# Kernel optimization log

Hardware: AMD Instinct MI355X
Metric: run time of the kernel (lower is better)

Reference implementation:

```python
import jax, jax.numpy as jnp
import numpy as np

T, B, N, E, NF, L = 4, 8, 5000, 80000, 16, 3


def setup_inputs() -> dict:
    key = jax.random.key(0)
    ks = jax.random.split(key, 12)
    xs = jax.random.normal(ks[0], (T, B, N, 3), jnp.float32)
    vs = jax.random.normal(ks[1], (T, B, N, 3), jnp.float32)
    charges = jax.random.uniform(ks[2], (B * N, 1), jnp.float32)
    edge_src = jax.random.randint(ks[3], (E,), 0, N)
    edge_dst = jax.random.randint(ks[4], (E,), 0, N)
    theta = jax.random.uniform(ks[5], (1, T), jnp.float32, -1.0, 1.0)  # uniform_(-1,1)
    W_embed = jax.random.normal(ks[6], (1, NF), jnp.float32) * 0.5
    W1 = jax.random.normal(ks[7], (L, 2 * NF + 1, NF), jnp.float32) / jnp.sqrt(2.0 * NF + 1)
    b1 = jnp.zeros((L, NF), jnp.float32)
    W2 = jax.random.normal(ks[8], (L, NF, NF), jnp.float32) / jnp.sqrt(float(NF))
    b2 = jnp.zeros((L, NF), jnp.float32)
    Wv = jax.random.normal(ks[9], (L, NF, 1), jnp.float32) * 0.1
    return dict(xs=xs, vs=vs, charges=charges, edge_src=edge_src, edge_dst=edge_dst,
                theta=theta, W_embed=W_embed, W1=W1, b1=b1, W2=W2, b2=b2, Wv=Wv)


def reference(xs, vs, charges, edge_src, edge_dst, theta, W_embed, W1, b1, W2, b2, Wv):
    T_, B_, N_, _ = xs.shape
    # node scalar features ('f' / type-0) initialized from charges
    h0 = jax.nn.relu(charges.reshape(B_, N_, 1) @ W_embed)  # [B, N, NF]

    def graph_step(x, v, h):
        # x, v: [N,3]; h: [N,NF]. Equivariant message passing with edge rel-pos gather.
        d = x[edge_dst] - x[edge_src]                      # [E,3]  (edata['d'])
        d2 = jnp.sum(d * d, axis=-1, keepdims=True)        # [E,1]  invariant edge feature
        vec = v                                            # type-1 ('vel') channel
        for l in range(L):
            feat = jnp.concatenate([h[edge_src], h[edge_dst], d2], axis=-1)  # [E,2NF+1]
            m = jax.nn.relu(feat @ W1[l] + b1[l])                            # [E,NF]
            agg = jax.ops.segment_sum(m, edge_dst, num_segments=N_)          # [N,NF]
            h = h + jax.nn.relu(agg @ W2[l] + b2[l])
            # equivariant vector update: scatter d-weighted messages
            vec = vec + jax.ops.segment_sum(d * (m @ Wv[l]), edge_dst, num_segments=N_)
        return vec + x  # module returns out + xs

    step_b = jax.vmap(graph_step)                                  # over batch
    out = jax.vmap(lambda x, v: step_b(x, v, h0))(xs, vs)          # [T,B,N,3]
    x = out.reshape(T_, B_ * N_, 3)                                # step's view(-1, 3)
    x_hat = jnp.einsum('ij,jkt->ikt', jax.nn.softmax(theta, axis=1), x)
    return x_hat.squeeze(0)  # [B*N, 3] since num_future == 1
```

## Files before the change

### kernel.cpp

```cpp
#include <hip/hip_runtime.h>
#include <hip/hip_bf16.h>

constexpr int T_ = 4;
constexpr int B_ = 8;
constexpr int N_ = 5000;
constexpr int E_ = 80000;
constexpr int TBN = T_ * B_ * N_;
constexpr int NXCD = 8;
constexpr int CAP = 64;

constexpr int NPB = 32;
constexpr int CH  = (N_ + NPB - 1) / NPB;
constexpr int GRP = T_ * B_ / NXCD;
constexpr int LB  = NXCD * CH * GRP;
constexpr int EB  = (E_ + 255) / 256;
constexpr int IB  = TBN / 256;


__device__ __forceinline__ unsigned bf16pack2(float lo, float hi) {
    unsigned ul = (__float_as_uint(lo) + 0x8000u) >> 16;
    unsigned uh = (__float_as_uint(hi) + 0x8000u) & 0xffff0000u;
    return uh | ul;
}
__device__ __forceinline__ void bf16unpack2(unsigned u, float& lo, float& hi) {
    lo = __uint_as_float(u << 16);
    hi = __uint_as_float(u & 0xffff0000u);
}

__global__ void k_build(const int* __restrict__ src, const int* __restrict__ dst,
                        int* __restrict__ cursor, unsigned short* __restrict__ csr_b,
                        const float* __restrict__ xs, const float* __restrict__ vs,
                        const float* __restrict__ charges,
                        float4* __restrict__ rec0, float4* __restrict__ rec1,
                        float* __restrict__ vec) {
    const int bid = blockIdx.x;
    const int tid = threadIdx.x;
    if (bid < EB) {
        int e = bid * 256 + tid;
        if (e < E_) {
            int d = dst[e];
            int pos = atomicAdd(&cursor[d], 1);
            if (pos < CAP) csr_b[d * CAP + pos] = (unsigned short)src[e];
        }
    } else {
        int g = (bid - EB) * 256 + tid;
        int tb = g / N_;
        int n  = g - tb * N_;
        int b  = tb % B_;
        float c = charges[b * N_ + n];
        float4 xc = make_float4(xs[3*(size_t)g], xs[3*(size_t)g+1], xs[3*(size_t)g+2], c);
        rec0[(size_t)g * 3 + 2] = xc;
        rec1[(size_t)g * 3 + 2] = xc;
        vec[3*(size_t)g+0] = vs[3*(size_t)g+0];
        vec[3*(size_t)g+1] = vs[3*(size_t)g+1];
        vec[3*(size_t)g+2] = vs[3*(size_t)g+2];
    }
}

template <int LYR, bool HAS_NEXT>
__global__ __launch_bounds__(256, 6) void k_layer(
        const float4* __restrict__ rec_in, float4* __restrict__ rec_out,
        const float* __restrict__ W_embed,
        const float* __restrict__ W1, const float* __restrict__ b1,
        const float* __restrict__ W2, const float* __restrict__ b2,
        const float* __restrict__ Wv, const float* __restrict__ theta,
        const int* __restrict__ degv, const unsigned short* __restrict__ csr_b,
        unsigned* __restrict__ hbuf, unsigned* __restrict__ gd,
        float* __restrict__ vec, float* __restrict__ outp) {
    __shared__ float s_w1e[16], s_wv[16], s_b2[16], s_b1[16], s_b1n[16];
    __shared__ float s_W2[256];
    __shared__ float s_W1sn[256];
    __shared__ float s_W1dn[256];
    __shared__ float s_P[16], s_Q[16], s_rwe[16];
    const int tid = threadIdx.x;
    if (tid < 16) {
        s_w1e[tid] = W1[LYR * 528 + 512 + tid];
        s_wv[tid]  = Wv[LYR * 16 + tid];
        s_b2[tid]  = b2[LYR * 16 + tid];
        s_b1[tid]  = b1[LYR * 16 + tid];
        if (HAS_NEXT) s_b1n[tid] = b1[(LYR + 1) * 16 + tid];
    }
    s_W2[tid] = W2[LYR * 256 + tid];
    if (HAS_NEXT) {
        s_W1sn[tid] = W1[(LYR + 1) * 528 + tid];
        s_W1dn[tid] = W1[(LYR + 1) * 528 + 256 + tid];
    }
    if (LYR == 0 && tid < 16) {
        float accP = 0.0f, accQ = 0.0f;
        for (int j = 0; j < 16; ++j) {
            float r = fmaxf(W_embed[j], 0.0f);
            accP += r * W1[j * 16 + tid];
            accQ += r * W1[256 + j * 16 + tid];
        }
        s_P[tid] = accP; s_Q[tid] = accQ;
        s_rwe[tid] = fmaxf(W_embed[tid], 0.0f);
    }
    __syncthreads();

    const int bid   = blockIdx.x;
    const int xcd   = bid & 7;
    const int j     = bid >> 3;
    const int tb    = xcd + NXCD * (j / CH);
    const int chunk = j % CH;
    const int o     = tid & 7;
    const int node  = chunk * NPB + (tid >> 3);
    const int half  = o & 1;
    const int pr    = o >> 1;
    const int hb    = half * 8;
    if (node >= N_) return;

    const int g = tb * N_ + node;
    const size_t nb = (size_t)tb * N_;
    const uint4* r4 = (const uint4*)rec_in;

    float wsm = 0.0f;
    if (!HAS_NEXT) {
        float t0 = theta[0], t1 = theta[1], t2 = theta[2], t3 = theta[3];
        float mx = fmaxf(fmaxf(t0, t1), fmaxf(t2, t3));
        float e0 = expf(t0 - mx), e1 = expf(t1 - mx);
        float e2 = expf(t2 - mx), e3 = expf(t3 - mx);
        float inv = 1.0f / (e0 + e1 + e2 + e3);
        int tt = tb >> 3;
        wsm = ((tt == 0) ? e0 : (tt == 1) ? e1 : (tt == 2) ? e2 : e3) * inv;
    }

    const float4 xn = rec_in[(size_t)g * 3 + 2];
    const float c0 = xn.w;

    float gdn[8];
    if (LYR == 0) {
#pragma unroll
        for (int k = 0; k < 8; ++k) gdn[k] = c0 * s_Q[hb + k] + s_b1[hb + k];
    } else {
        uint4 da = ((const uint4*)gd)[(size_t)g * 2 + half];
        bf16unpack2(da.x, gdn[0], gdn[1]);  bf16unpack2(da.y, gdn[2], gdn[3]);
        bf16unpack2(da.z, gdn[4], gdn[5]);  bf16unpack2(da.w, gdn[6], gdn[7]);
    }

    float agg[8];
#pragma unroll
    for (int k = 0; k < 8; ++k) agg[k] = 0.0f;
    float av0 = 0.0f, av1 = 0.0f, av2 = 0.0f;

    const int deg = min(degv[node], CAP);
    const int rs = node * CAP;
    const int re = rs + deg;

    int e = rs + pr;
    bool have = e < re;
    int s = have ? (int)csr_b[e] : 0;
    size_t si = nb + (size_t)s;
    float4 xc = rec_in[si * 3 + 2];
    uint4  ga;
    if (LYR != 0) ga = r4[si * 3 + half];

    while (have) {
        int e2 = e + 4;
        bool have2 = e2 < re;
        int s2 = have2 ? (int)csr_b[e2] : 0;
        size_t si2 = nb + (size_t)s2;
        float4 xc2 = rec_in[si2 * 3 + 2];
        uint4  ga2;
        if (LYR != 0) ga2 = r4[si2 * 3 + half];

        float d0 = xn.x - xc.x;
        float d1 = xn.y - xc.y;
        float d2v = xn.z - xc.z;
        float dd = d0*d0 + d1*d1 + d2v*d2v;

        float gsf[8];
        if (LYR == 0) {
            float cs = xc.w;
#pragma unroll
            for (int k = 0; k < 8; ++k) gsf[k] = cs * s_P[hb + k];
        } else {
            bf16unpack2(ga.x, gsf[0], gsf[1]);  bf16unpack2(ga.y, gsf[2], gsf[3]);
            bf16unpack2(ga.z, gsf[4], gsf[5]);  bf16unpack2(ga.w, gsf[6], gsf[7]);
        }

        float sval = 0.0f;
#pragma unroll
        for (int k = 0; k < 8; ++k) {
            float mv = fmaxf(__builtin_fmaf(dd, s_w1e[hb + k], gdn[k]) + gsf[k], 0.0f);
            if (HAS_NEXT) agg[k] += mv;
            sval = __builtin_fmaf(mv, s_wv[hb + k], sval);
        }
        sval += __shfl_xor(sval, 1);
        av0 = __builtin_fmaf(d0, sval, av0);
        av1 = __builtin_fmaf(d1, sval, av1);
        av2 = __builtin_fmaf(d2v, sval, av2);

        e = e2; have = have2; xc = xc2; ga = ga2;
    }

    av0 += __shfl_xor(av0, 2); av0 += __shfl_xor(av0, 4);
    av1 += __shfl_xor(av1, 2); av1 += __shfl_xor(av1, 4);
    av2 += __shfl_xor(av2, 2); av2 += __shfl_xor(av2, 4);

    if (HAS_NEXT) {
        if (o < 3) {
            float myav = (o == 0) ? av0 : ((o == 1) ? av1 : av2);
            vec[(size_t)g * 3 + o] += myav;
        }

#pragma unroll
        for (int k = 0; k < 8; ++k) {
            agg[k] += __shfl_xor(agg[k], 2);
            agg[k] += __shfl_xor(agg[k], 4);
        }
        float aggO[8];
#pragma unroll
        for (int k = 0; k < 8; ++k) aggO[k] = __shfl_xor(agg[k], 1);
        const int j0 = hb;
        const int j1 = 8 - hb;

        float hq0, hq1;
        if (LYR == 0) {
            hq0 = c0 * s_rwe[o * 2];
            hq1 = c0 * s_rwe[o * 2 + 1];
        } else {
            bf16unpack2(hbuf[(size_t)g * 8 + o], hq0, hq1);
        }

        float a0 = s_b2[o * 2], a1 = s_b2[o * 2 + 1];
#pragma unroll
        for (int k = 0; k < 8; ++k) {
            a0 = __builtin_fmaf(agg[k],  s_W2[(j0 + k) * 16 + o * 2],     a0);
            a1 = __builtin_fmaf(agg[k],  s_W2[(j0 + k) * 16 + o * 2 + 1], a1);
            a0 = __builtin_fmaf(aggO[k], s_W2[(j1 + k) * 16 + o * 2],     a0);
            a1 = __builtin_fmaf(aggO[k], s_W2[(j1 + k) * 16 + o * 2 + 1], a1);
        }
        hq0 += fmaxf(a0, 0.0f);
        hq1 += fmaxf(a1, 0.0f);

        const int lane = tid & 63;
        const int lbase = lane & ~7;
        float hfull[16];
#pragma unroll
        for (int sq = 0; sq < 8; ++sq) {
            hfull[sq * 2]     = __shfl(hq0, lbase + sq, 64);
            hfull[sq * 2 + 1] = __shfl(hq1, lbase + sq, 64);
        }

        float gs0 = 0.0f, gs1 = 0.0f;
        float gd0 = s_b1n[o * 2], gd1 = s_b1n[o * 2 + 1];
#pragma unroll
        for (int jj = 0; jj < 16; ++jj) {
            float hj = hfull[jj];
            gs0 = __builtin_fmaf(hj, s_W1sn[jj * 16 + o * 2],     gs0);
            gs1 = __builtin_fmaf(hj, s_W1sn[jj * 16 + o * 2 + 1], gs1);
            gd0 = __builtin_fmaf(hj, s_W1dn[jj * 16 + o * 2],     gd0);
            gd1 = __builtin_fmaf(hj, s_W1dn[jj * 16 + o * 2 + 1], gd1);
        }

        hbuf[(size_t)g * 8 + o] = bf16pack2(hq0, hq1);
        ((unsigned*)rec_out)[(size_t)g * 12 + o] = bf16pack2(gs0, gs1);
        ((unsigned*)gd)[(size_t)g * 8 + o]       = bf16pack2(gd0, gd1);
    } else {
        if (o < 3) {
            float myav = (o == 0) ? av0 : ((o == 1) ? av1 : av2);
            float xno  = (o == 0) ? xn.x : ((o == 1) ? xn.y : xn.z);
            float prev = vec[(size_t)g * 3 + o];
            int b = tb & 7;
            atomicAdd(&outp[((size_t)b * N_ + node) * 3 + o],
                      wsm * (prev + myav + xno));
        }
    }
}

extern "C" void kernel_launch(void* const* d_in, const int* in_sizes, int n_in,
                              void* d_out, int out_size, void* d_ws, size_t ws_size,
                              hipStream_t stream) {
    const float* xs       = (const float*)d_in[0];
    const float* vs       = (const float*)d_in[1];
    const float* charges  = (const float*)d_in[2];
    const int*   edge_src = (const int*)d_in[3];
    const int*   edge_dst = (const int*)d_in[4];
    const float* theta    = (const float*)d_in[5];
    const float* W_embed  = (const float*)d_in[6];
    const float* W1       = (const float*)d_in[7];
    const float* b1       = (const float*)d_in[8];
    const float* W2       = (const float*)d_in[9];
    const float* b2       = (const float*)d_in[10];
    const float* Wv       = (const float*)d_in[11];
    float* out = (float*)d_out;

    char* w = (char*)d_ws;
    size_t off = 0;
    auto take = [&](size_t bytes) {
        size_t o = off;
        off = (off + bytes + 255) & ~(size_t)255;
        return o;
    };
    int*            cursor = (int*)(w + take((size_t)N_ * 4));
    unsigned short* csr_b  = (unsigned short*)(w + take((size_t)N_ * CAP * 2));
    float4*         rec0   = (float4*)(w + take((size_t)TBN * 48));
    float4*         rec1   = (float4*)(w + take((size_t)TBN * 48));
    unsigned*       hbuf   = (unsigned*)(w + take((size_t)TBN * 32));
    unsigned*       gd     = (unsigned*)(w + take((size_t)TBN * 32));
    float*          vec    = (float*)(w + take((size_t)TBN * 3 * 4));
    (void)ws_size;

    hipMemsetAsync(cursor, 0, (size_t)N_ * 4, stream);
    hipMemsetAsync(out, 0, (size_t)out_size * 4, stream);
    k_build<<<EB + IB, 256, 0, stream>>>(edge_src, edge_dst, cursor, csr_b,
                                         xs, vs, charges, rec0, rec1, vec);

    k_layer<0, true ><<<LB, 256, 0, stream>>>(rec0, rec1, W_embed, W1, b1, W2, b2, Wv,
                                              theta, cursor, csr_b, hbuf, gd, vec, out);
    k_layer<1, true ><<<LB, 256, 0, stream>>>(rec1, rec0, W_embed, W1, b1, W2, b2, Wv,
                                              theta, cursor, csr_b, hbuf, gd, vec, out);
    k_layer<2, false><<<LB, 256, 0, stream>>>(rec0, nullptr, W_embed, W1, b1, W2, b2, Wv,
                                              theta, cursor, csr_b, hbuf, gd, vec, out);
}
```

Measured before the change: 106.8 us.

## Quantize positions/charges to int16 and stage whole graph in LDS

Positions and charges are quantized once into 8-byte fixed-point records. Each layer block copies all 5000 node records for its graph into shared memory, so neighbor position gathers read LDS instead of global memory. The gs records shrink from a 48-byte interleaved layout to a separate 32-byte array, and blocks grow to 512 threads handling 64 nodes each. The trade-offs are fixed-point precision loss on positions, about 40KB of LDS per block that limits occupancy, and a per-block load of the whole graph that is repeated across chunks.

```diff
diff --git a/kernel.cpp b/kernel.cpp
--- a/kernel.cpp
+++ b/kernel.cpp
@@ -9,13 +9,18 @@
 constexpr int NXCD = 8;
 constexpr int CAP = 64;
 
-constexpr int NPB = 32;
+constexpr int TPB = 512;
+constexpr int NPB = 64;
 constexpr int CH  = (N_ + NPB - 1) / NPB;
 constexpr int GRP = T_ * B_ / NXCD;
 constexpr int LB  = NXCD * CH * GRP;
 constexpr int EB  = (E_ + 255) / 256;
 constexpr int IB  = TBN / 256;
 
+constexpr float QS  = 4096.0f;
+constexpr float IQS = 1.0f / 4096.0f;
+constexpr float QC  = 16384.0f;
+constexpr float IQC = 1.0f / 16384.0f;
 
 __device__ __forceinline__ unsigned bf16pack2(float lo, float hi) {
     unsigned ul = (__float_as_uint(lo) + 0x8000u) >> 16;
@@ -26,13 +31,19 @@
     lo = __uint_as_float(u << 16);
     hi = __uint_as_float(u & 0xffff0000u);
 }
+__device__ __forceinline__ void unpackq(uint2 p, float& x, float& y, float& z,
+                                        float& c) {
+    x = (float)(short)(p.x & 0xffffu) * IQS;
+    y = (float)(short)(p.x >> 16)     * IQS;
+    z = (float)(short)(p.y & 0xffffu) * IQS;
+    c = (float)(p.y >> 16)            * IQC;
+}
 
 __global__ void k_build(const int* __restrict__ src, const int* __restrict__ dst,
                         int* __restrict__ cursor, unsigned short* __restrict__ csr_b,
                         const float* __restrict__ xs, const float* __restrict__ vs,
                         const float* __restrict__ charges,
-                        float4* __restrict__ rec0, float4* __restrict__ rec1,
-                        float* __restrict__ vec) {
+                        uint2* __restrict__ xcq, float* __restrict__ vec) {
     const int bid = blockIdx.x;
     const int tid = threadIdx.x;
     if (bid < EB) {
@@ -48,9 +59,16 @@
         int n  = g - tb * N_;
         int b  = tb % B_;
         float c = charges[b * N_ + n];
-        float4 xc = make_float4(xs[3*(size_t)g], xs[3*(size_t)g+1], xs[3*(size_t)g+2], c);
-        rec0[(size_t)g * 3 + 2] = xc;
-        rec1[(size_t)g * 3 + 2] = xc;
+        int qx = __float2int_rn(xs[3*(size_t)g]   * QS);
+        int qy = __float2int_rn(xs[3*(size_t)g+1] * QS);
+        int qz = __float2int_rn(xs[3*(size_t)g+2] * QS);
+        int qc = __float2int_rn(c * QC);
+        qx = max(-32768, min(32767, qx));
+        qy = max(-32768, min(32767, qy));
+        qz = max(-32768, min(32767, qz));
+        qc = max(0, min(65535, qc));
+        xcq[g] = make_uint2((qx & 0xffff) | ((unsigned)(qy & 0xffff) << 16),
+                            (qz & 0xffff) | ((unsigned)qc << 16));
         vec[3*(size_t)g+0] = vs[3*(size_t)g+0];
         vec[3*(size_t)g+1] = vs[3*(size_t)g+1];
         vec[3*(size_t)g+2] = vs[3*(size_t)g+2];
@@ -58,8 +76,9 @@
 }
 
 template <int LYR, bool HAS_NEXT>
-__global__ __launch_bounds__(256, 6) void k_layer(
-        const float4* __restrict__ rec_in, float4* __restrict__ rec_out,
+__global__ __launch_bounds__(TPB, 6) void k_layer(
+        const uint2* __restrict__ xcq, const uint4* __restrict__ gs_in,
+        unsigned* __restrict__ gs_out,
         const float* __restrict__ W_embed,
         const float* __restrict__ W1, const float* __restrict__ b1,
         const float* __restrict__ W2, const float* __restrict__ b2,
@@ -67,6 +86,7 @@
         const int* __restrict__ degv, const unsigned short* __restrict__ csr_b,
         unsigned* __restrict__ hbuf, unsigned* __restrict__ gd,
         float* __restrict__ vec, float* __restrict__ outp) {
+    __shared__ uint2 sxq[N_];
     __shared__ float s_w1e[16], s_wv[16], s_b2[16], s_b1[16], s_b1n[16];
     __shared__ float s_W2[256];
     __shared__ float s_W1sn[256];
@@ -80,10 +100,12 @@
         s_b1[tid]  = b1[LYR * 16 + tid];
         if (HAS_NEXT) s_b1n[tid] = b1[(LYR + 1) * 16 + tid];
     }
-    s_W2[tid] = W2[LYR * 256 + tid];
-    if (HAS_NEXT) {
-        s_W1sn[tid] = W1[(LYR + 1) * 528 + tid];
-        s_W1dn[tid] = W1[(LYR + 1) * 528 + 256 + tid];
+    if (tid < 256) {
+        s_W2[tid] = W2[LYR * 256 + tid];
+        if (HAS_NEXT) {
+            s_W1sn[tid] = W1[(LYR + 1) * 528 + tid];
+            s_W1dn[tid] = W1[(LYR + 1) * 528 + 256 + tid];
+        }
     }
     if (LYR == 0 && tid < 16) {
         float accP = 0.0f, accQ = 0.0f;
@@ -95,13 +117,17 @@
         s_P[tid] = accP; s_Q[tid] = accQ;
         s_rwe[tid] = fmaxf(W_embed[tid], 0.0f);
     }
-    __syncthreads();
 
     const int bid   = blockIdx.x;
     const int xcd   = bid & 7;
     const int j     = bid >> 3;
     const int tb    = xcd + NXCD * (j / CH);
     const int chunk = j % CH;
+    const size_t nb = (size_t)tb * N_;
+
+    for (int i = tid; i < N_; i += TPB) sxq[i] = xcq[nb + i];
+    __syncthreads();
+
     const int o     = tid & 7;
     const int node  = chunk * NPB + (tid >> 3);
     const int half  = o & 1;
@@ -110,8 +136,6 @@
     if (node >= N_) return;
 
     const int g = tb * N_ + node;
-    const size_t nb = (size_t)tb * N_;
-    const uint4* r4 = (const uint4*)rec_in;
 
     float wsm = 0.0f;
     if (!HAS_NEXT) {
@@ -124,8 +148,8 @@
         wsm = ((tt == 0) ? e0 : (tt == 1) ? e1 : (tt == 2) ? e2 : e3) * inv;
     }
 
-    const float4 xn = rec_in[(size_t)g * 3 + 2];
-    const float c0 = xn.w;
+    float xn0, xn1, xn2, c0;
+    unpackq(sxq[node], xn0, xn1, xn2, c0);
 
     float gdn[8];
     if (LYR == 0) {
@@ -149,28 +173,25 @@
     int e = rs + pr;
     bool have = e < re;
     int s = have ? (int)csr_b[e] : 0;
-    size_t si = nb + (size_t)s;
-    float4 xc = rec_in[si * 3 + 2];
-    uint4  ga;
-    if (LYR != 0) ga = r4[si * 3 + half];
+    uint4 ga;
+    if (LYR != 0) ga = gs_in[(nb + (size_t)s) * 2 + half];
 
     while (have) {
         int e2 = e + 4;
         bool have2 = e2 < re;
         int s2 = have2 ? (int)csr_b[e2] : 0;
-        size_t si2 = nb + (size_t)s2;
-        float4 xc2 = rec_in[si2 * 3 + 2];
-        uint4  ga2;
-        if (LYR != 0) ga2 = r4[si2 * 3 + half];
-
-        float d0 = xn.x - xc.x;
-        float d1 = xn.y - xc.y;
-        float d2v = xn.z - xc.z;
+        uint4 ga2;
+        if (LYR != 0) ga2 = gs_in[(nb + (size_t)s2) * 2 + half];
+
+        float xc0, xc1, xc2, cs;
+        unpackq(sxq[s], xc0, xc1, xc2, cs);
+        float d0 = xn0 - xc0;
+        float d1 = xn1 - xc1;
+        float d2v = xn2 - xc2;
         float dd = d0*d0 + d1*d1 + d2v*d2v;
 
         float gsf[8];
         if (LYR == 0) {
-            float cs = xc.w;
 #pragma unroll
             for (int k = 0; k < 8; ++k) gsf[k] = cs * s_P[hb + k];
         } else {
@@ -190,7 +211,7 @@
         av1 = __builtin_fmaf(d1, sval, av1);
         av2 = __builtin_fmaf(d2v, sval, av2);
 
-        e = e2; have = have2; xc = xc2; ga = ga2;
+        e = e2; have = have2; s = s2; ga = ga2;
     }
 
     av0 += __shfl_xor(av0, 2); av0 += __shfl_xor(av0, 4);
@@ -253,13 +274,13 @@
             gd1 = __builtin_fmaf(hj, s_W1dn[jj * 16 + o * 2 + 1], gd1);
         }
 
-        hbuf[(size_t)g * 8 + o] = bf16pack2(hq0, hq1);
-        ((unsigned*)rec_out)[(size_t)g * 12 + o] = bf16pack2(gs0, gs1);
-        ((unsigned*)gd)[(size_t)g * 8 + o]       = bf16pack2(gd0, gd1);
+        hbuf[(size_t)g * 8 + o]   = bf16pack2(hq0, hq1);
+        gs_out[(size_t)g * 8 + o] = bf16pack2(gs0, gs1);
+        ((unsigned*)gd)[(size_t)g * 8 + o] = bf16pack2(gd0, gd1);
     } else {
         if (o < 3) {
             float myav = (o == 0) ? av0 : ((o == 1) ? av1 : av2);
-            float xno  = (o == 0) ? xn.x : ((o == 1) ? xn.y : xn.z);
+            float xno  = (o == 0) ? xn0 : ((o == 1) ? xn1 : xn2);
             float prev = vec[(size_t)g * 3 + o];
             int b = tb & 7;
             atomicAdd(&outp[((size_t)b * N_ + node) * 3 + o],
@@ -294,8 +315,9 @@
     };
     int*            cursor = (int*)(w + take((size_t)N_ * 4));
     unsigned short* csr_b  = (unsigned short*)(w + take((size_t)N_ * CAP * 2));
-    float4*         rec0   = (float4*)(w + take((size_t)TBN * 48));
-    float4*         rec1   = (float4*)(w + take((size_t)TBN * 48));
+    uint2*          xcq    = (uint2*)(w + take((size_t)TBN * 8));
+    unsigned*       gsA    = (unsigned*)(w + take((size_t)TBN * 32));
+    unsigned*       gsB    = (unsigned*)(w + take((size_t)TBN * 32));
     unsigned*       hbuf   = (unsigned*)(w + take((size_t)TBN * 32));
     unsigned*       gd     = (unsigned*)(w + take((size_t)TBN * 32));
     float*          vec    = (float*)(w + take((size_t)TBN * 3 * 4));
@@ -304,12 +326,15 @@
     hipMemsetAsync(cursor, 0, (size_t)N_ * 4, stream);
     hipMemsetAsync(out, 0, (size_t)out_size * 4, stream);
     k_build<<<EB + IB, 256, 0, stream>>>(edge_src, edge_dst, cursor, csr_b,
-                                         xs, vs, charges, rec0, rec1, vec);
-
-    k_layer<0, true ><<<LB, 256, 0, stream>>>(rec0, rec1, W_embed, W1, b1, W2, b2, Wv,
-                                              theta, cursor, csr_b, hbuf, gd, vec, out);
-    k_layer<1, true ><<<LB, 256, 0, stream>>>(rec1, rec0, W_embed, W1, b1, W2, b2, Wv,
-                                              theta, cursor, csr_b, hbuf, gd, vec, out);
-    k_layer<2, false><<<LB, 256, 0, stream>>>(rec0, nullptr, W_embed, W1, b1, W2, b2, Wv,
-                                              theta, cursor, csr_b, hbuf, gd, vec, out);
-}
+                                         xs, vs, charges, xcq, vec);
+
+    k_layer<0, true ><<<LB, TPB, 0, stream>>>(xcq, nullptr, gsA,
+                                              W_embed, W1, b1, W2, b2, Wv, theta,
+                                              cursor, csr_b, hbuf, gd, vec, out);
+    k_layer<1, true ><<<LB, TPB, 0, stream>>>(xcq, (const uint4*)gsA, gsB,
+                                              W_embed, W1, b1, W2, b2, Wv, theta,
+                                              cursor, csr_b, hbuf, gd, vec, out);
+    k_layer<2, false><<<LB, TPB, 0, stream>>>(xcq, (const uint4*)gsB, nullptr,
+                                              W_embed, W1, b1, W2, b2, Wv, theta,
+                                              cursor, csr_b, hbuf, gd, vec, out);
+}
```

Result: slower. 115.8 us (+8.4%).

## Switch edge-message math and stored node features from bf16/fp32 to packed fp16

Applied to the files above, without the earlier changes.

Stored node features (h, gs, gd) change from bf16 to fp16 so they can feed packed half2 arithmetic directly. The per-edge message loop now runs as packed fp16 ops (pk_fma, pk_max, pk_add) on pairs of channels, and aggregation and its cross-lane shuffle reductions are also done in fp16. This roughly halves the VALU instruction count in the hot edge loop and removes the bf16 unpack shifts. The cost is reduced precision and range: fp16 accumulation over up to 64 edges and squared distances cast to fp16 could overflow or lose accuracy.

```diff
diff --git a/kernel.cpp b/kernel.cpp
--- a/kernel.cpp
+++ b/kernel.cpp
@@ -17,14 +17,19 @@
 constexpr int IB  = TBN / 256;
 
 
-__device__ __forceinline__ unsigned bf16pack2(float lo, float hi) {
-    unsigned ul = (__float_as_uint(lo) + 0x8000u) >> 16;
-    unsigned uh = (__float_as_uint(hi) + 0x8000u) & 0xffff0000u;
-    return uh | ul;
-}
-__device__ __forceinline__ void bf16unpack2(unsigned u, float& lo, float& hi) {
-    lo = __uint_as_float(u << 16);
-    hi = __uint_as_float(u & 0xffff0000u);
+typedef _Float16 h2 __attribute__((ext_vector_type(2)));
+__device__ __forceinline__ unsigned h2u(h2 v) {
+    union { h2 h; unsigned u; } x; x.h = v; return x.u;
+}
+__device__ __forceinline__ h2 u2h(unsigned u) {
+    union { h2 h; unsigned u; } x; x.u = u; return x.h;
+}
+__device__ __forceinline__ unsigned f16pack2(float lo, float hi) {
+    auto v = __builtin_amdgcn_cvt_pkrtz(lo, hi);
+    union { decltype(v) h; unsigned u; } x; x.h = v; return x.u;
+}
+__device__ __forceinline__ void f16unpack2(unsigned u, float& lo, float& hi) {
+    h2 v = u2h(u); lo = (float)v[0]; hi = (float)v[1];
 }
 
 __global__ void k_build(const int* __restrict__ src, const int* __restrict__ dst,
@@ -127,19 +132,28 @@
     const float4 xn = rec_in[(size_t)g * 3 + 2];
     const float c0 = xn.w;
 
-    float gdn[8];
+    h2 w1e_pk[4], wv_pk[4], P_pk[4];
+#pragma unroll
+    for (int k = 0; k < 4; ++k) {
+        w1e_pk[k] = u2h(f16pack2(s_w1e[hb + 2*k], s_w1e[hb + 2*k + 1]));
+        wv_pk[k]  = u2h(f16pack2(s_wv[hb + 2*k],  s_wv[hb + 2*k + 1]));
+        if (LYR == 0) P_pk[k] = u2h(f16pack2(s_P[hb + 2*k], s_P[hb + 2*k + 1]));
+    }
+
+    h2 gdn_pk[4];
     if (LYR == 0) {
 #pragma unroll
-        for (int k = 0; k < 8; ++k) gdn[k] = c0 * s_Q[hb + k] + s_b1[hb + k];
+        for (int k = 0; k < 4; ++k)
+            gdn_pk[k] = u2h(f16pack2(c0 * s_Q[hb + 2*k]     + s_b1[hb + 2*k],
+                                     c0 * s_Q[hb + 2*k + 1] + s_b1[hb + 2*k + 1]));
     } else {
         uint4 da = ((const uint4*)gd)[(size_t)g * 2 + half];
-        bf16unpack2(da.x, gdn[0], gdn[1]);  bf16unpack2(da.y, gdn[2], gdn[3]);
-        bf16unpack2(da.z, gdn[4], gdn[5]);  bf16unpack2(da.w, gdn[6], gdn[7]);
-    }
-
-    float agg[8];
-#pragma unroll
-    for (int k = 0; k < 8; ++k) agg[k] = 0.0f;
+        gdn_pk[0] = u2h(da.x); gdn_pk[1] = u2h(da.y);
+        gdn_pk[2] = u2h(da.z); gdn_pk[3] = u2h(da.w);
+    }
+
+    const h2 h2z = {(_Float16)0.0f, (_Float16)0.0f};
+    h2 agg_pk[4] = {h2z, h2z, h2z, h2z};
     float av0 = 0.0f, av1 = 0.0f, av2 = 0.0f;
 
     const int deg = min(degv[node], CAP);
@@ -167,24 +181,23 @@
         float d1 = xn.y - xc.y;
         float d2v = xn.z - xc.z;
         float dd = d0*d0 + d1*d1 + d2v*d2v;
-
-        float gsf[8];
-        if (LYR == 0) {
-            float cs = xc.w;
-#pragma unroll
-            for (int k = 0; k < 8; ++k) gsf[k] = cs * s_P[hb + k];
-        } else {
-            bf16unpack2(ga.x, gsf[0], gsf[1]);  bf16unpack2(ga.y, gsf[2], gsf[3]);
-            bf16unpack2(ga.z, gsf[4], gsf[5]);  bf16unpack2(ga.w, gsf[6], gsf[7]);
-        }
-
-        float sval = 0.0f;
-#pragma unroll
-        for (int k = 0; k < 8; ++k) {
-            float mv = fmaxf(__builtin_fmaf(dd, s_w1e[hb + k], gdn[k]) + gsf[k], 0.0f);
-            if (HAS_NEXT) agg[k] += mv;
-            sval = __builtin_fmaf(mv, s_wv[hb + k], sval);
-        }
+        _Float16 ddh = (_Float16)dd;
+        h2 dd2 = {ddh, ddh};
+        h2 cs2 = h2z;
+        if (LYR == 0) { _Float16 ch = (_Float16)xc.w; cs2 = (h2){ch, ch}; }
+
+        h2 sv = h2z;
+#pragma unroll
+        for (int k = 0; k < 4; ++k) {
+            h2 gsk;
+            if (LYR == 0) gsk = cs2 * P_pk[k];
+            else gsk = u2h(k == 0 ? ga.x : (k == 1 ? ga.y : (k == 2 ? ga.z : ga.w)));
+            h2 m = dd2 * w1e_pk[k] + gdn_pk[k] + gsk;
+            m = __builtin_elementwise_max(m, h2z);
+            if (HAS_NEXT) agg_pk[k] += m;
+            sv = m * wv_pk[k] + sv;
+        }
+        float sval = (float)sv[0] + (float)sv[1];
         sval += __shfl_xor(sval, 1);
         av0 = __builtin_fmaf(d0, sval, av0);
         av1 = __builtin_fmaf(d1, sval, av1);
@@ -203,14 +216,16 @@
             vec[(size_t)g * 3 + o] += myav;
         }
 
-#pragma unroll
-        for (int k = 0; k < 8; ++k) {
-            agg[k] += __shfl_xor(agg[k], 2);
-            agg[k] += __shfl_xor(agg[k], 4);
-        }
-        float aggO[8];
-#pragma unroll
-        for (int k = 0; k < 8; ++k) aggO[k] = __shfl_xor(agg[k], 1);
+        float agg[8], aggO[8];
+#pragma unroll
+        for (int k = 0; k < 4; ++k) {
+            agg_pk[k] += u2h(__shfl_xor(h2u(agg_pk[k]), 2));
+            agg_pk[k] += u2h(__shfl_xor(h2u(agg_pk[k]), 4));
+            unsigned po = __shfl_xor(h2u(agg_pk[k]), 1);
+            h2 v = agg_pk[k], vo = u2h(po);
+            agg[2*k]   = (float)v[0];  agg[2*k+1]  = (float)v[1];
+            aggO[2*k]  = (float)vo[0]; aggO[2*k+1] = (float)vo[1];
+        }
         const int j0 = hb;
         const int j1 = 8 - hb;
 
@@ -219,7 +234,7 @@
             hq0 = c0 * s_rwe[o * 2];
             hq1 = c0 * s_rwe[o * 2 + 1];
         } else {
-            bf16unpack2(hbuf[(size_t)g * 8 + o], hq0, hq1);
+            f16unpack2(hbuf[(size_t)g * 8 + o], hq0, hq1);
         }
 
         float a0 = s_b2[o * 2], a1 = s_b2[o * 2 + 1];
@@ -253,9 +268,9 @@
             gd1 = __builtin_fmaf(hj, s_W1dn[jj * 16 + o * 2 + 1], gd1);
         }
 
-        hbuf[(size_t)g * 8 + o] = bf16pack2(hq0, hq1);
-        ((unsigned*)rec_out)[(size_t)g * 12 + o] = bf16pack2(gs0, gs1);
-        ((unsigned*)gd)[(size_t)g * 8 + o]       = bf16pack2(gd0, gd1);
+        hbuf[(size_t)g * 8 + o] = f16pack2(hq0, hq1);
+        ((unsigned*)rec_out)[(size_t)g * 12 + o] = f16pack2(gs0, gs1);
+        ((unsigned*)gd)[(size_t)g * 8 + o]       = f16pack2(gd0, gd1);
     } else {
         if (o < 3) {
             float myav = (o == 0) ? av0 : ((o == 1) ? av1 : av2);
```

Result: faster. 100.1 us (median of 2 runs) (-6.2%).
